# Kernel optimization log

Measured on AMD Instinct MI355X. Metric: run time of the kernel, lower is better.

The kernel has to match this reference:

```python
import jax, jax.numpy as jnp
from jax import lax
import numpy as np

B, T, C = 4, 1024, 1024
NH, HS = 16, 64
K, STRIDE = 32, 16
EPS = 1e-5


def _ln(x, w, b):
    m = jnp.mean(x, axis=-1, keepdims=True)
    v = jnp.mean((x - m) ** 2, axis=-1, keepdims=True)
    return (x - m) * lax.rsqrt(v + EPS) * w + b


def setup_inputs() -> dict:
    key = jax.random.key(0)
    ks = jax.random.split(key, 12)
    s = 0.02
    return {
        'x': jax.random.normal(ks[0], (B, T, C), jnp.float32),
        'c_attn_w': jax.random.normal(ks[1], (C, 3 * C), jnp.float32) * s,
        'c_attn_b': jnp.zeros((3 * C,), jnp.float32),
        'c_proj_w': jax.random.normal(ks[2], (C, C), jnp.float32) * s,
        'c_proj_b': jnp.zeros((C,), jnp.float32),
        'conv_w': jax.random.normal(ks[3], (HS, HS, K), jnp.float32) * s,  # OIH
        'conv_b': jnp.zeros((HS,), jnp.float32),
        'comp_ln_w': jnp.ones((HS,), jnp.float32),
        'comp_ln_b': jnp.zeros((HS,), jnp.float32),
        'ln_local_w': jnp.ones((C,), jnp.float32),
        'ln_local_b': jnp.zeros((C,), jnp.float32),
        'gate_w1': jax.random.normal(ks[4], (2 * C, C), jnp.float32) * s,
        'gate_b1': jnp.zeros((C,), jnp.float32),
        'gate_ln_w': jnp.ones((C,), jnp.float32),
        'gate_ln_b': jnp.zeros((C,), jnp.float32),
        'gate_w2': jax.random.normal(ks[5], (C, 2), jnp.float32) * s,
        'gate_b2': jnp.zeros((2,), jnp.float32),
    }


def _compress(h, conv_w, conv_b, comp_ln_w, comp_ln_b):
    # h: [B, nh, T, hs] -> [B, nh, num_blocks, hs]
    b, nh, t, hs = h.shape
    xr = h.transpose(0, 1, 3, 2).reshape(b * nh, hs, t)  # NCH
    co = lax.conv_general_dilated(xr, conv_w, (STRIDE,), 'VALID',
                                  dimension_numbers=('NCH', 'OIH', 'NCH'))
    co = co + conv_b[None, :, None]
    y = co.transpose(0, 2, 1)  # [B*nh, nb, hs]
    y = _ln(y, comp_ln_w, comp_ln_b)
    y = jax.nn.gelu(y, approximate=False)
    return y.reshape(b, nh, -1, hs)


def _attn(q, k, v, mask):
    # q:[B,nh,T,hs] k,v:[B,nh,Tk,hs], mask:[T,Tk] bool (True=keep)
    scale = 1.0 / jnp.sqrt(jnp.asarray(q.shape[-1], q.dtype))
    att = jnp.einsum('bhqd,bhkd->bhqk', q, k) * scale
    att = jnp.where(mask[None, None], att, jnp.finfo(att.dtype).min)
    att = jax.nn.softmax(att, axis=-1)
    return jnp.einsum('bhqk,bhkd->bhqd', att, v)


def reference(x, c_attn_w, c_attn_b, c_proj_w, c_proj_b, conv_w, conv_b,
              comp_ln_w, comp_ln_b, ln_local_w, ln_local_b,
              gate_w1, gate_b1, gate_ln_w, gate_ln_b, gate_w2, gate_b2):
    b, t, c = x.shape
    qkv = x @ c_attn_w + c_attn_b
    q, k, v = jnp.split(qkv, 3, axis=-1)
    q = q.reshape(b, t, NH, HS).transpose(0, 2, 1, 3)
    k = k.reshape(b, t, NH, HS).transpose(0, 2, 1, 3)
    v = v.reshape(b, t, NH, HS).transpose(0, 2, 1, 3)

    k_comp = _compress(k, conv_w, conv_b, comp_ln_w, comp_ln_b)
    v_comp = _compress(v, conv_w, conv_b, comp_ln_w, comp_ln_b)
    nb = k_comp.shape[2]

    # local branch: flash path with is_causal=True skips the window mask -> plain causal
    causal = jnp.tril(jnp.ones((t, t), bool))
    local = _attn(q, k, v, causal)
    local = local.transpose(0, 2, 1, 3).reshape(b, t, c)
    local_norm = _ln(local, ln_local_w, ln_local_b)

    # compressed branch: causal mask of shape [T, num_blocks], diagonal 0
    comp_mask = jnp.tril(jnp.ones((t, nb), bool), k=0)
    comp = _attn(q, k_comp, v_comp, comp_mask)
    comp = comp.transpose(0, 2, 1, 3).reshape(b, t, c)

    # gating from last-token features
    feats = jnp.concatenate([local_norm[:, -1, :], comp[:, -1, :]], axis=-1)  # [B, 2C]
    h = jax.nn.relu(_ln(feats @ gate_w1 + gate_b1, gate_ln_w, gate_ln_b))
    gates = jax.nn.softmax(h @ gate_w2 + gate_b2, axis=-1)  # [B, 2]
    g = gates[:, None, :]  # [B, 1, 2]
    combined = g[..., 0:1] * local_norm + g[..., 1:2] * comp

    return combined @ c_proj_w + c_proj_b
```

## Files before the change

### kernel.cpp

```cpp
#include <hip/hip_runtime.h>

using u16 = unsigned short;
using f32x4 = __attribute__((ext_vector_type(4))) float;
using s16x8 = __attribute__((ext_vector_type(8))) short;
using u16x4 = __attribute__((ext_vector_type(4))) unsigned short;

__device__ __forceinline__ u16 f2bf(float f) {
  unsigned u = __float_as_uint(f);
  return (u16)((u + 0x7FFFu + ((u >> 16) & 1u)) >> 16);
}

__device__ __forceinline__ f32x4 mfma16(s16x8 a, s16x8 b, f32x4 c) {
  return __builtin_amdgcn_mfma_f32_16x16x32_bf16(a, b, c, 0, 0, 0);
}

__device__ __forceinline__ void gld16(const void* g, void* l) {
  __builtin_amdgcn_global_load_lds(
      (const __attribute__((address_space(1))) unsigned int*)g,
      (__attribute__((address_space(3))) unsigned int*)l, 16, 0, 0);
}

__global__ __launch_bounds__(256) void cast_bf16(const float* __restrict__ in,
                                                 u16* __restrict__ out, int n4) {
  int i = blockIdx.x * 256 + threadIdx.x;
  if (i >= n4) return;
  f32x4 v = *(const f32x4*)(in + (size_t)i * 4);
  u16x4 o = {f2bf(v[0]), f2bf(v[1]), f2bf(v[2]), f2bf(v[3])};
  *(u16x4*)(out + (size_t)i * 4) = o;
}

__global__ __launch_bounds__(256) void transpose_cast(const float* __restrict__ in,
                                                      u16* __restrict__ out,
                                                      int R, int C) {
  __shared__ float t[32][33];
  int bx = blockIdx.x, by = blockIdx.y;
  int tx = threadIdx.x & 31, ty = threadIdx.x >> 5;
#pragma unroll
  for (int r = 0; r < 4; r++) {
    int row = by * 32 + ty + r * 8;
    t[ty + r * 8][tx] = in[(size_t)row * C + bx * 32 + tx];
  }
  __syncthreads();
#pragma unroll
  for (int r = 0; r < 4; r++) {
    int orow = bx * 32 + ty + r * 8;
    out[(size_t)orow * R + by * 32 + tx] = f2bf(t[tx][ty + r * 8]);
  }
}

__device__ __forceinline__ void gemm_mainloop(const u16* A, const u16* Bt, int K,
                                              u16* As, u16* Bs, f32x4 acc[4][4]) {
  const int tid = threadIdx.x;
  const int row = tid >> 2, c16 = tid & 3;
  const int lane = tid & 63, wid = tid >> 6;
  const int wm = wid >> 1, wn = wid & 1, lg = lane >> 4, lr = lane & 15;
  const u16* ga = A + (size_t)row * K + c16 * 8;
  const u16* gb = Bt + (size_t)row * K + c16 * 8;
  const size_t rowskip = (size_t)64 * K;
  for (int k0 = 0; k0 < K; k0 += 32) {
    gld16(ga + k0, As + tid * 8);
    gld16(ga + rowskip + k0, As + 2048 + tid * 8);
    gld16(gb + k0, Bs + tid * 8);
    gld16(gb + rowskip + k0, Bs + 2048 + tid * 8);
    __syncthreads();
    s16x8 af[4], bfr[4];
#pragma unroll
    for (int i = 0; i < 4; i++)
      af[i] = *(const s16x8*)(As + (wm * 64 + i * 16 + lr) * 32 + lg * 8);
#pragma unroll
    for (int j = 0; j < 4; j++)
      bfr[j] = *(const s16x8*)(Bs + (wn * 64 + j * 16 + lr) * 32 + lg * 8);
#pragma unroll
    for (int i = 0; i < 4; i++)
#pragma unroll
      for (int j = 0; j < 4; j++) acc[i][j] = mfma16(af[i], bfr[j], acc[i][j]);
    __syncthreads();
  }
}

__global__ __launch_bounds__(256) void gemm_qkv(const u16* __restrict__ A,
                                                const u16* __restrict__ Bt,
                                                const float* __restrict__ bias,
                                                u16* __restrict__ qo, u16* __restrict__ ko,
                                                u16* __restrict__ kTo, u16* __restrict__ vTo) {
  __shared__ u16 As[4096];
  __shared__ u16 Bs[4096];
  int m0 = blockIdx.x * 128, n0 = blockIdx.y * 128;
  f32x4 acc[4][4] = {};
  gemm_mainloop(A + (size_t)m0 * 1024, Bt + (size_t)n0 * 1024, 1024, As, Bs, acc);
  int lane = threadIdx.x & 63, wid = threadIdx.x >> 6;
  int wm = wid >> 1, wn = wid & 1, lg = lane >> 4, lr = lane & 15;
#pragma unroll
  for (int i = 0; i < 4; i++) {
    int mb = m0 + wm * 64 + i * 16 + lg * 4;
    int b = mb >> 10, tb = mb & 1023;
#pragma unroll
    for (int j = 0; j < 4; j++) {
      int n = n0 + wn * 64 + j * 16 + lr;
      float bs = bias[n];
      int sel = n >> 10, hd = n & 1023, h = hd >> 6, d = hd & 63;
      int bh = b * 16 + h;
      u16 u0 = f2bf(acc[i][j][0] + bs), u1 = f2bf(acc[i][j][1] + bs);
      u16 u2 = f2bf(acc[i][j][2] + bs), u3 = f2bf(acc[i][j][3] + bs);
      if (sel == 0) {
        u16* qp = qo + ((size_t)bh << 16) + ((size_t)tb << 6) + d;
        qp[0] = u0; qp[64] = u1; qp[128] = u2; qp[192] = u3;
      } else if (sel == 1) {
        u16* kp = ko + ((size_t)bh << 16) + ((size_t)tb << 6) + d;
        kp[0] = u0; kp[64] = u1; kp[128] = u2; kp[192] = u3;
        u16x4 pk = {u0, u1, u2, u3};
        *(u16x4*)(kTo + ((size_t)(bh * 64 + d) << 10) + tb) = pk;
      } else {
        u16x4 pk = {u0, u1, u2, u3};
        *(u16x4*)(vTo + ((size_t)(bh * 64 + d) << 10) + tb) = pk;
      }
    }
  }
}

__global__ __launch_bounds__(256) void gemm_proj(const u16* __restrict__ A,
                                                 const u16* __restrict__ Bt,
                                                 const float* __restrict__ bias,
                                                 float* __restrict__ out) {
  __shared__ u16 As[4096];
  __shared__ u16 Bs[4096];
  int m0 = blockIdx.x * 128, n0 = blockIdx.y * 128;
  f32x4 acc[4][4] = {};
  gemm_mainloop(A + (size_t)m0 * 1024, Bt + (size_t)n0 * 1024, 1024, As, Bs, acc);
  int lane = threadIdx.x & 63, wid = threadIdx.x >> 6;
  int wm = wid >> 1, wn = wid & 1, lg = lane >> 4, lr = lane & 15;
#pragma unroll
  for (int i = 0; i < 4; i++) {
    int mb = m0 + wm * 64 + i * 16 + lg * 4;
#pragma unroll
    for (int j = 0; j < 4; j++) {
      int n = n0 + wn * 64 + j * 16 + lr;
      float bs = bias[n];
#pragma unroll
      for (int r = 0; r < 4; r++)
        out[(size_t)(mb + r) * 1024 + n] = acc[i][j][r] + bs;
    }
  }
}

__global__ __launch_bounds__(256) void conv_comp(const u16* __restrict__ kT,
                                                 const u16* __restrict__ vT,
                                                 const u16* __restrict__ cw,
                                                 const float* __restrict__ cb,
                                                 const float* __restrict__ lnw,
                                                 const float* __restrict__ lnb,
                                                 u16* __restrict__ kcomp,
                                                 u16* __restrict__ vcompT) {
  int bh = blockIdx.x, sel = blockIdx.y;
  const u16* src = (sel ? vT : kT) + ((size_t)bh << 16);
  int tid = threadIdx.x, wid = tid >> 6, lane = tid & 63, lg = lane >> 4, lr = lane & 15;
  f32x4 acc[4] = {};
  int arow = wid * 16 + lr;
  if (arow > 62) arow = 62;
  const u16* abase = src + (size_t)arow * 16 + lg * 8;
#pragma unroll 4
  for (int ic = 0; ic < 64; ic++) {
    s16x8 a = *(const s16x8*)(abase + ic * 1024);
#pragma unroll
    for (int j = 0; j < 4; j++) {
      s16x8 bfr = *(const s16x8*)(cw + (size_t)(j * 16 + lr) * 2048 + ic * 32 + lg * 8);
      acc[j] = mfma16(a, bfr, acc[j]);
    }
  }
  float lwv[4], lbv[4];
#pragma unroll
  for (int j = 0; j < 4; j++) {
    int oc = j * 16 + lr;
    float cbv = cb[oc];
    acc[j][0] += cbv; acc[j][1] += cbv; acc[j][2] += cbv; acc[j][3] += cbv;
    lwv[j] = lnw[oc]; lbv[j] = lnb[oc];
  }
#pragma unroll
  for (int r = 0; r < 4; r++) {
    float s = acc[0][r] + acc[1][r] + acc[2][r] + acc[3][r];
    float q = acc[0][r] * acc[0][r] + acc[1][r] * acc[1][r] +
              acc[2][r] * acc[2][r] + acc[3][r] * acc[3][r];
#pragma unroll
    for (int off = 1; off < 16; off <<= 1) {
      s += __shfl_xor(s, off);
      q += __shfl_xor(q, off);
    }
    float mean = s * (1.f / 64.f);
    float var = q * (1.f / 64.f) - mean * mean;
    float rstd = rsqrtf(fmaxf(var, 0.f) + 1e-5f);
    int op = wid * 16 + lg * 4 + r;
#pragma unroll
    for (int j = 0; j < 4; j++) {
      float y = (acc[j][r] - mean) * rstd * lwv[j] + lbv[j];
      y = 0.5f * y * (1.0f + erff(y * 0.70710678118f));
      if (op > 62) y = 0.f;
      int oc = j * 16 + lr;
      if (sel == 0) kcomp[((size_t)bh << 12) + (op << 6) + oc] = f2bf(y);
      else          vcompT[((size_t)bh << 12) + (oc << 6) + op] = f2bf(y);
    }
  }
}

__global__ __launch_bounds__(256) void flash64(const u16* __restrict__ qg,
                                               const u16* __restrict__ kg,
                                               const u16* __restrict__ vg,
                                               float* __restrict__ outg,
                                               int k_bh, int v_bh, int vrow, int kvmax) {
  __shared__ u16 Pl[4][1152];
  const int tid = threadIdx.x;
  const int w = tid >> 6, lane = tid & 63, lg = lane >> 4, lr = lane & 15;
  const int idx = blockIdx.x;
  const int nqt = gridDim.x >> 6;
  const int xcd = idx & 7, j = idx >> 3;
  const int bh = xcd * 8 + (j & 7);
  const int qt0 = nqt - 1 - (j >> 3);
  const int q0 = qt0 * 64;
  const int qrow = q0 + w * 16 + lr;
  const u16* qb = qg + ((size_t)bh << 16) + (size_t)qrow * 64 + lg * 8;
  s16x8 qf0 = *(const s16x8*)(qb);
  s16x8 qf1 = *(const s16x8*)(qb + 32);
  const u16* kb = kg + (size_t)bh * k_bh;
  const u16* vb = vg + (size_t)bh * v_bh;
  int nt = qt0 + 1;
  int ntk = (kvmax + 63) >> 6;
  if (nt > ntk) nt = ntk;
  u16* Pw = Pl[w];
  f32x4 ot[4] = {};
  float m = -INFINITY, l = 0.f;
  const float SCL = 0.125f * 1.44269504089f;
  for (int t = 0; t < nt; t++) {
    const int kv0 = t * 64;
    const bool full = (kv0 + 63 <= q0 + w * 16) && (kv0 + 64 <= kvmax);
    f32x4 st[4];
    __builtin_amdgcn_s_setprio(1);
#pragma unroll
    for (int kvt = 0; kvt < 4; kvt++) {
      const u16* ka = kb + (size_t)(kv0 + kvt * 16 + lr) * 64 + lg * 8;
      f32x4 z = {};
      z = mfma16(*(const s16x8*)(ka), qf0, z);
      z = mfma16(*(const s16x8*)(ka + 32), qf1, z);
      st[kvt] = z;
    }
    __builtin_amdgcn_s_setprio(0);
    float p[16];
    float tm = -INFINITY;
    if (full) {
#pragma unroll
      for (int kvt = 0; kvt < 4; kvt++)
#pragma unroll
        for (int r = 0; r < 4; r++) {
          float v = st[kvt][r] * SCL;
          p[kvt * 4 + r] = v;
          tm = fmaxf(tm, v);
        }
    } else {
#pragma unroll
      for (int kvt = 0; kvt < 4; kvt++)
#pragma unroll
        for (int r = 0; r < 4; r++) {
          int kvi = kv0 + kvt * 16 + lg * 4 + r;
          float v = st[kvt][r] * SCL;
          v = (kvi <= qrow && kvi < kvmax) ? v : -INFINITY;
          p[kvt * 4 + r] = v;
          tm = fmaxf(tm, v);
        }
    }
    tm = fmaxf(tm, __shfl_xor(tm, 16));
    tm = fmaxf(tm, __shfl_xor(tm, 32));
    if (!__all(tm <= m)) {
      float mnew = fmaxf(m, tm);
      float fac = exp2f(m - mnew);
      l *= fac;
#pragma unroll
      for (int d4 = 0; d4 < 4; d4++) {
        ot[d4][0] *= fac; ot[d4][1] *= fac; ot[d4][2] *= fac; ot[d4][3] *= fac;
      }
      m = mnew;
    }
    float ls = 0.f;
#pragma unroll
    for (int i = 0; i < 16; i++) {
      float e = exp2f(p[i] - m);
      p[i] = e;
      ls += e;
    }
    ls += __shfl_xor(ls, 16);
    ls += __shfl_xor(ls, 32);
    l += ls;
#pragma unroll
    for (int kvt = 0; kvt < 4; kvt++) {
      unsigned w0 = (unsigned)f2bf(p[kvt * 4 + 0]) | ((unsigned)f2bf(p[kvt * 4 + 1]) << 16);
      unsigned w1 = (unsigned)f2bf(p[kvt * 4 + 2]) | ((unsigned)f2bf(p[kvt * 4 + 3]) << 16);
      uint2 pk = {w0, w1};
      *(uint2*)(Pw + lr * 72 + kvt * 16 + lg * 4) = pk;
    }
    s16x8 bp0 = *(const s16x8*)(Pw + lr * 72 + lg * 8);
    s16x8 bp1 = *(const s16x8*)(Pw + lr * 72 + 32 + lg * 8);
    __builtin_amdgcn_s_setprio(1);
#pragma unroll
    for (int d4 = 0; d4 < 4; d4++) {
      const u16* va = vb + (size_t)(d4 * 16 + lr) * vrow + kv0 + lg * 8;
      ot[d4] = mfma16(*(const s16x8*)(va), bp0, ot[d4]);
      ot[d4] = mfma16(*(const s16x8*)(va + 32), bp1, ot[d4]);
    }
    __builtin_amdgcn_s_setprio(0);
  }
  float inv = 1.f / l;
  int b = bh >> 4, h = bh & 15;
  float* op = outg + ((size_t)((b << 10) + qrow) << 10) + h * 64;
#pragma unroll
  for (int d4 = 0; d4 < 4; d4++) {
    f32x4 v;
#pragma unroll
    for (int c = 0; c < 4; c++) v[c] = ot[d4][c] * inv;
    *(f32x4*)(op + d4 * 16 + lg * 4) = v;
  }
}

__global__ __launch_bounds__(256) void ln_rows(float* __restrict__ x,
                                               const float* __restrict__ w,
                                               const float* __restrict__ b) {
  __shared__ float red[8];
  size_t row = blockIdx.x;
  float* xr = x + (row << 10);
  int tid = threadIdx.x;
  f32x4 v = *(const f32x4*)(xr + tid * 4);
  float s = v[0] + v[1] + v[2] + v[3];
  float q = v[0] * v[0] + v[1] * v[1] + v[2] * v[2] + v[3] * v[3];
#pragma unroll
  for (int off = 32; off >= 1; off >>= 1) {
    s += __shfl_xor(s, off);
    q += __shfl_xor(q, off);
  }
  int wid = tid >> 6;
  if ((tid & 63) == 0) { red[wid * 2] = s; red[wid * 2 + 1] = q; }
  __syncthreads();
  s = red[0] + red[2] + red[4] + red[6];
  q = red[1] + red[3] + red[5] + red[7];
  float mean = s * (1.0f / 1024.0f);
  float var = q * (1.0f / 1024.0f) - mean * mean;
  float rstd = rsqrtf(fmaxf(var, 0.f) + 1e-5f);
  f32x4 wv = *(const f32x4*)(w + tid * 4);
  f32x4 bv = *(const f32x4*)(b + tid * 4);
  f32x4 o;
#pragma unroll
  for (int c = 0; c < 4; c++) o[c] = (v[c] - mean) * rstd * wv[c] + bv[c];
  *(f32x4*)(xr + tid * 4) = o;
}

__global__ __launch_bounds__(256) void gate_partial(const float* __restrict__ ln,
                                                    const float* __restrict__ comp,
                                                    const float* __restrict__ w1,
                                                    float* __restrict__ partial) {
  __shared__ float f[4][32];
  int ib = blockIdx.x, i0 = ib * 32, tid = threadIdx.x;
  if (tid < 128) {
    int bb = tid >> 5, ii = tid & 31;
    int i = i0 + ii;
    const float* src = (i < 1024) ? ln : comp;
    int ic = i & 1023;
    f[bb][ii] = src[((size_t)(bb * 1024 + 1023) << 10) + ic];
  }
  __syncthreads();
  float acc[4][4] = {};
  for (int ii = 0; ii < 32; ii++) {
    float f0 = f[0][ii], f1 = f[1][ii], f2 = f[2][ii], f3 = f[3][ii];
#pragma unroll
    for (int jj = 0; jj < 4; jj++) {
      float w = w1[(size_t)(i0 + ii) * 1024 + jj * 256 + tid];
      acc[jj][0] += f0 * w; acc[jj][1] += f1 * w;
      acc[jj][2] += f2 * w; acc[jj][3] += f3 * w;
    }
  }
#pragma unroll
  for (int jj = 0; jj < 4; jj++)
#pragma unroll
    for (int bb = 0; bb < 4; bb++)
      partial[(size_t)((ib << 2) + bb) * 1024 + jj * 256 + tid] = acc[jj][bb];
}

__global__ __launch_bounds__(1024) void gate_finish(const float* __restrict__ partial,
                                                    const float* __restrict__ b1,
                                                    const float* __restrict__ lnw,
                                                    const float* __restrict__ lnb,
                                                    const float* __restrict__ w2,
                                                    const float* __restrict__ b2,
                                                    float* __restrict__ g) {
  __shared__ float redA[16], redB[16];
  int b = blockIdx.x, j = threadIdx.x;
  float s = b1[j];
#pragma unroll 4
  for (int ib = 0; ib < 64; ib++) s += partial[(size_t)((ib << 2) + b) * 1024 + j];
  float sa = s, sb = s * s;
#pragma unroll
  for (int off = 32; off >= 1; off >>= 1) {
    sa += __shfl_xor(sa, off);
    sb += __shfl_xor(sb, off);
  }
  int wid = j >> 6;
  if ((j & 63) == 0) { redA[wid] = sa; redB[wid] = sb; }
  __syncthreads();
  if (j == 0) {
    float A = 0, Bv = 0;
    for (int k2 = 0; k2 < 16; k2++) { A += redA[k2]; Bv += redB[k2]; }
    redA[0] = A; redB[0] = Bv;
  }
  __syncthreads();
  float S = redA[0], Q = redB[0];
  float mean = S * (1.f / 1024.f), var = Q * (1.f / 1024.f) - mean * mean;
  float rstd = rsqrtf(fmaxf(var, 0.f) + 1e-5f);
  float hn = (s - mean) * rstd * lnw[j] + lnb[j];
  hn = fmaxf(hn, 0.f);
  float c0 = hn * w2[j * 2], c1 = hn * w2[j * 2 + 1];
  __syncthreads();
  float ra = c0, rb = c1;
#pragma unroll
  for (int off = 32; off >= 1; off >>= 1) {
    ra += __shfl_xor(ra, off);
    rb += __shfl_xor(rb, off);
  }
  if ((j & 63) == 0) { redA[wid] = ra; redB[wid] = rb; }
  __syncthreads();
  if (j == 0) {
    float A = 0, Bv = 0;
    for (int k2 = 0; k2 < 16; k2++) { A += redA[k2]; Bv += redB[k2]; }
    A += b2[0]; Bv += b2[1];
    float mx = fmaxf(A, Bv);
    float e0 = __expf(A - mx), e1 = __expf(Bv - mx);
    float inv = 1.f / (e0 + e1);
    g[b * 2] = e0 * inv;
    g[b * 2 + 1] = e1 * inv;
  }
}

__global__ __launch_bounds__(256) void combine_k(const float* __restrict__ ln,
                                                 const float* __restrict__ comp,
                                                 const float* __restrict__ g,
                                                 u16* __restrict__ out) {
  size_t i = (size_t)blockIdx.x * 256 + threadIdx.x;
  size_t off = i << 2;
  int b = (int)(off >> 20);
  float g0 = g[b * 2], g1 = g[b * 2 + 1];
  f32x4 a = *(const f32x4*)(ln + off);
  f32x4 c = *(const f32x4*)(comp + off);
  u16x4 o = {f2bf(g0 * a[0] + g1 * c[0]), f2bf(g0 * a[1] + g1 * c[1]),
             f2bf(g0 * a[2] + g1 * c[2]), f2bf(g0 * a[3] + g1 * c[3])};
  *(u16x4*)(out + off) = o;
}

extern "C" void kernel_launch(void* const* d_in, const int* in_sizes, int n_in,
                              void* d_out, int out_size, void* d_ws, size_t ws_size,
                              hipStream_t stream) {
  const float* x        = (const float*)d_in[0];
  const float* c_attn_w = (const float*)d_in[1];
  const float* c_attn_b = (const float*)d_in[2];
  const float* c_proj_w = (const float*)d_in[3];
  const float* c_proj_b = (const float*)d_in[4];
  const float* conv_w   = (const float*)d_in[5];
  const float* conv_b   = (const float*)d_in[6];
  const float* comp_ln_w= (const float*)d_in[7];
  const float* comp_ln_b= (const float*)d_in[8];
  const float* ln_loc_w = (const float*)d_in[9];
  const float* ln_loc_b = (const float*)d_in[10];
  const float* gate_w1  = (const float*)d_in[11];
  const float* gate_b1  = (const float*)d_in[12];
  const float* gate_ln_w= (const float*)d_in[13];
  const float* gate_ln_b= (const float*)d_in[14];
  const float* gate_w2  = (const float*)d_in[15];
  const float* gate_b2  = (const float*)d_in[16];
  float* out = (float*)d_out;

  char* ws = (char*)d_ws;
  size_t off = 0;
  auto alloc = [&](size_t bytes) -> char* {
    char* p = ws + off;
    off += (bytes + 255) & ~(size_t)255;
    return p;
  };
  u16* x_bf     = (u16*)alloc(8388608);
  u16* attn_wT  = (u16*)alloc(6291456);
  u16* proj_wT  = (u16*)alloc(2097152);
  u16* conv_wbf = (u16*)alloc(262144);
  u16* q_bf     = (u16*)alloc(8388608);
  u16* k_bf     = (u16*)alloc(8388608);
  u16* kT_bf    = (u16*)alloc(8388608);
  u16* vT_bf    = (u16*)alloc(8388608);
  u16* k_comp   = (u16*)alloc(524288);
  u16* v_compT  = (u16*)alloc(524288);
  float* local  = (float*)alloc(16777216);
  float* comp   = (float*)alloc(16777216);
  float* partial= (float*)alloc(1048576);
  float* gbuf   = (float*)alloc(256);
  u16* combined = x_bf;
  if (off > ws_size) return;

  cast_bf16<<<dim3(4096), dim3(256), 0, stream>>>(x, x_bf, 1048576);
  transpose_cast<<<dim3(96, 32), dim3(256), 0, stream>>>(c_attn_w, attn_wT, 1024, 3072);
  transpose_cast<<<dim3(32, 32), dim3(256), 0, stream>>>(c_proj_w, proj_wT, 1024, 1024);
  cast_bf16<<<dim3(128), dim3(256), 0, stream>>>(conv_w, conv_wbf, 32768);

  gemm_qkv<<<dim3(32, 24), dim3(256), 0, stream>>>(x_bf, attn_wT, c_attn_b,
                                                   q_bf, k_bf, kT_bf, vT_bf);

  conv_comp<<<dim3(64, 2), dim3(256), 0, stream>>>(kT_bf, vT_bf, conv_wbf, conv_b,
                                                   comp_ln_w, comp_ln_b, k_comp, v_compT);

  flash64<<<dim3(1024), dim3(256), 0, stream>>>(q_bf, k_bf, vT_bf, local,
                                                65536, 65536, 1024, 1024);
  flash64<<<dim3(1024), dim3(256), 0, stream>>>(q_bf, k_comp, v_compT, comp,
                                                4096, 4096, 64, 63);

  ln_rows<<<dim3(4096), dim3(256), 0, stream>>>(local, ln_loc_w, ln_loc_b);

  gate_partial<<<dim3(64), dim3(256), 0, stream>>>(local, comp, gate_w1, partial);
  gate_finish<<<dim3(4), dim3(1024), 0, stream>>>(partial, gate_b1, gate_ln_w,
                                                  gate_ln_b, gate_w2, gate_b2, gbuf);

  combine_k<<<dim3(4096), dim3(256), 0, stream>>>(local, comp, gbuf, combined);
  gemm_proj<<<dim3(32, 8), dim3(256), 0, stream>>>(combined, proj_wT, c_proj_b, out);
}
```

Baseline: 334.1 us.

## Double-buffer K tiles in LDS and prefetch V fragments in flash64

Each K tile is now staged into a swizzled, double-buffered LDS array using async global-to-LDS loads, so the next tile's load overlaps the current tile's compute. Previously every wave read K directly from global memory, and all four waves re-read the same rows. V fragments are also loaded into registers early in each iteration to hide their latency before the PV MFMAs. The launch bounds gain an occupancy hint. The cost is more LDS use, a block-wide barrier every iteration, and higher register pressure from the V prefetch.

```diff
diff --git a/kernel.cpp b/kernel.cpp
--- a/kernel.cpp
+++ b/kernel.cpp
@@ -201,11 +201,12 @@
   }
 }
 
-__global__ __launch_bounds__(256) void flash64(const u16* __restrict__ qg,
-                                               const u16* __restrict__ kg,
-                                               const u16* __restrict__ vg,
-                                               float* __restrict__ outg,
-                                               int k_bh, int v_bh, int vrow, int kvmax) {
+__global__ __launch_bounds__(256, 4) void flash64(const u16* __restrict__ qg,
+                                                  const u16* __restrict__ kg,
+                                                  const u16* __restrict__ vg,
+                                                  float* __restrict__ outg,
+                                                  int k_bh, int v_bh, int vrow, int kvmax) {
+  __shared__ u16 Ks[2][4096];
   __shared__ u16 Pl[4][1152];
   const int tid = threadIdx.x;
   const int w = tid >> 6, lane = tid & 63, lg = lane >> 4, lr = lane & 15;
@@ -228,20 +229,47 @@
   f32x4 ot[4] = {};
   float m = -INFINITY, l = 0.f;
   const float SCL = 0.125f * 1.44269504089f;
+
+  auto stageK = [&](int bufi, int kv0) {
+#pragma unroll
+    for (int rnd = 0; rnd < 2; rnd++) {
+      int o = tid * 16 + rnd * 4096;
+      int row = o >> 7;
+      int sb = (o & 127) ^ ((row & 7) << 4);
+      gld16(kb + (size_t)(kv0 + row) * 64 + (sb >> 1), &Ks[bufi][o >> 1]);
+    }
+  };
+
+  stageK(0, 0);
+  int cur = 0;
   for (int t = 0; t < nt; t++) {
+    __syncthreads();
+    if (t + 1 < nt) stageK(cur ^ 1, (t + 1) * 64);
     const int kv0 = t * 64;
+    const u16* Kb = Ks[cur];
     const bool full = (kv0 + 63 <= q0 + w * 16) && (kv0 + 64 <= kvmax);
+    s16x8 vlo[4];
+#pragma unroll
+    for (int d4 = 0; d4 < 4; d4++)
+      vlo[d4] = *(const s16x8*)(vb + (size_t)(d4 * 16 + lr) * vrow + kv0 + lg * 8);
     f32x4 st[4];
     __builtin_amdgcn_s_setprio(1);
 #pragma unroll
     for (int kvt = 0; kvt < 4; kvt++) {
-      const u16* ka = kb + (size_t)(kv0 + kvt * 16 + lr) * 64 + lg * 8;
+      int rr = kvt * 16 + lr;
+      int sw = (rr & 7) << 4;
+      s16x8 k0 = *(const s16x8*)(Kb + (((rr << 7) + ((lg * 16) ^ sw)) >> 1));
+      s16x8 k1 = *(const s16x8*)(Kb + (((rr << 7) + ((64 + lg * 16) ^ sw)) >> 1));
       f32x4 z = {};
-      z = mfma16(*(const s16x8*)(ka), qf0, z);
-      z = mfma16(*(const s16x8*)(ka + 32), qf1, z);
+      z = mfma16(k0, qf0, z);
+      z = mfma16(k1, qf1, z);
       st[kvt] = z;
     }
     __builtin_amdgcn_s_setprio(0);
+    s16x8 vhi[4];
+#pragma unroll
+    for (int d4 = 0; d4 < 4; d4++)
+      vhi[d4] = *(const s16x8*)(vb + (size_t)(d4 * 16 + lr) * vrow + kv0 + 32 + lg * 8);
     float p[16];
     float tm = -INFINITY;
     if (full) {
@@ -299,11 +327,11 @@
     __builtin_amdgcn_s_setprio(1);
 #pragma unroll
     for (int d4 = 0; d4 < 4; d4++) {
-      const u16* va = vb + (size_t)(d4 * 16 + lr) * vrow + kv0 + lg * 8;
-      ot[d4] = mfma16(*(const s16x8*)(va), bp0, ot[d4]);
-      ot[d4] = mfma16(*(const s16x8*)(va + 32), bp1, ot[d4]);
+      ot[d4] = mfma16(vlo[d4], bp0, ot[d4]);
+      ot[d4] = mfma16(vhi[d4], bp1, ot[d4]);
     }
     __builtin_amdgcn_s_setprio(0);
+    cur ^= 1;
   }
   float inv = 1.f / l;
   int b = bh >> 4, h = bh & 15;
```

New measurement: 301.6 us. 1.11x faster.
